# Kernel optimization log

Measured on AMD Instinct MI355X. Metric: run time of the kernel, lower is better.

Reference implementation:

```python
import jax, jax.numpy as jnp
import numpy as np

ALPHA = 0.9        # LIF membrane decay
THRESH = 1.0       # spike threshold
SURR_BETA = 4.0    # surrogate-gradient sharpness
TIME_STEPS = 32    # fabric simulation steps per token position


def _spike(v):
    """Heaviside spike with sigmoid surrogate gradient (straight-through)."""
    hard = (v >= THRESH).astype(v.dtype)
    soft = jax.nn.sigmoid(SURR_BETA * (v - THRESH))
    return soft + jax.lax.stop_gradient(hard - soft)


def setup_inputs() -> dict:
    key = jax.random.key(0)
    k0, k1, k2, k3 = jax.random.split(key, 4)
    B, S, D = 8, 128, 512
    N_in, N_out = 1024, 1024
    embeddings = jax.random.normal(k0, (B, S, D), jnp.float32)
    W_in = jax.random.normal(k1, (D, N_in), jnp.float32) / np.sqrt(D).astype(np.float32)
    b_in = jnp.zeros((N_in,), jnp.float32)
    W_conn = jax.random.normal(k2, (N_in, N_out), jnp.float32) / np.sqrt(N_in).astype(np.float32)
    W_out = jax.random.normal(k3, (N_out, D), jnp.float32) / np.sqrt(N_out).astype(np.float32)
    b_out = jnp.zeros((D,), jnp.float32)
    return {"embeddings": embeddings, "W_in": W_in, "b_in": b_in,
            "W_conn": W_conn, "W_out": W_out, "b_out": b_out}


def reference(embeddings, W_in, b_in, W_conn, W_out, b_out):
    B, S, D = embeddings.shape
    N_in = W_in.shape[1]
    N_out = W_conn.shape[1]

    # embed_to_snn + relu, precomputed for all positions: [B, S, N_in]
    snn_input = jax.nn.relu(jnp.einsum('bsd,dn->bsn', embeddings, W_in) + b_in)

    def time_step(carry, _):
        v_in, v_out, pos_input = carry
        # input population: leaky integrate external current
        v_in = ALPHA * v_in + pos_input
        s_in = _spike(v_in)
        v_in = v_in - s_in * THRESH          # soft reset
        # output population: driven by input-population spikes
        v_out = ALPHA * v_out + s_in @ W_conn
        s_out = _spike(v_out)
        v_out = v_out - s_out * THRESH
        n_spk = jax.lax.stop_gradient(s_in.sum() + s_out.sum())
        return (v_in, v_out, pos_input), (s_out, n_spk)

    def pos_step(carry, pos_input):
        v_in, v_out = carry
        (v_in, v_out, _), (s_outs, n_spks) = jax.lax.scan(
            time_step, (v_in, v_out, pos_input), None, length=TIME_STEPS)
        spike_acc = s_outs.sum(axis=0)       # [B, N_out], sum over timesteps
        pos_out = spike_acc @ W_out + b_out  # snn_to_embed
        return (v_in, v_out), (pos_out, n_spks.sum())

    v0_in = jnp.zeros((B, N_in), embeddings.dtype)
    v0_out = jnp.zeros((B, N_out), embeddings.dtype)
    snn_seq = jnp.swapaxes(snn_input, 0, 1)  # [S, B, N_in]: scan over positions
    _, (outs, spk_counts) = jax.lax.scan(pos_step, (v0_in, v0_out), snn_seq)

    output_embeddings = jnp.swapaxes(outs, 0, 1)  # [B, S, D]
    total_neurons = N_in + N_out
    spike_rate = spk_counts.sum() / (B * S * total_neurons * TIME_STEPS)
    return output_embeddings, spike_rate
```

## Files before the change

kernel.cpp:

```cpp
#include <hip/hip_runtime.h>
#include <stdint.h>

#define B 8
#define S 128
#define D 512
#define NIN 1024
#define NOUT 1024
#define T 32

typedef __attribute__((ext_vector_type(8))) short short8;
typedef __attribute__((ext_vector_type(4))) float floatx4;

__device__ __forceinline__ void gload_lds16(const void* g, void* l)
{
    __builtin_amdgcn_global_load_lds(
        (const __attribute__((address_space(1))) unsigned int*)g,
        (__attribute__((address_space(3))) unsigned int*)l,
        16, 0, 0);
}

__global__ __launch_bounds__(256) void k_gemm(const float* __restrict__ A,
                                              const float* __restrict__ Bm,
                                              const float* __restrict__ bias,
                                              float* __restrict__ C,
                                              int M, int N, int K, int relu)
{
    __shared__ float As[16][64];
    __shared__ float Bs[16][64];
    const int tid = threadIdx.x;
    const int bx = blockIdx.x, by = blockIdx.y;
    const int tx = tid & 15, ty = tid >> 4;
    const int ar = tid >> 2, ak = (tid & 3) << 2;
    const int bk = tid >> 4, bc = (tid & 15) << 2;
    float acc[4][4] = {{0.f,0.f,0.f,0.f},{0.f,0.f,0.f,0.f},
                       {0.f,0.f,0.f,0.f},{0.f,0.f,0.f,0.f}};
    float4 a4 = *(const float4*)(A + (size_t)(by*64 + ar)*K + ak);
    float4 b4 = *(const float4*)(Bm + (size_t)bk*N + bx*64 + bc);
    for (int k0 = 0; k0 < K; k0 += 16) {
        __syncthreads();
        As[ak+0][ar] = a4.x; As[ak+1][ar] = a4.y;
        As[ak+2][ar] = a4.z; As[ak+3][ar] = a4.w;
        *(float4*)&Bs[bk][bc] = b4;
        float4 na, nb;
        const bool has = (k0 + 16 < K);
        if (has) {
            na = *(const float4*)(A + (size_t)(by*64 + ar)*K + k0 + 16 + ak);
            nb = *(const float4*)(Bm + (size_t)(k0 + 16 + bk)*N + bx*64 + bc);
        }
        __syncthreads();
        #pragma unroll
        for (int kk = 0; kk < 16; ++kk) {
            float4 av = *(const float4*)&As[kk][ty << 2];
            float4 bv = *(const float4*)&Bs[kk][tx << 2];
            acc[0][0] = fmaf(av.x, bv.x, acc[0][0]);
            acc[0][1] = fmaf(av.x, bv.y, acc[0][1]);
            acc[0][2] = fmaf(av.x, bv.z, acc[0][2]);
            acc[0][3] = fmaf(av.x, bv.w, acc[0][3]);
            acc[1][0] = fmaf(av.y, bv.x, acc[1][0]);
            acc[1][1] = fmaf(av.y, bv.y, acc[1][1]);
            acc[1][2] = fmaf(av.y, bv.z, acc[1][2]);
            acc[1][3] = fmaf(av.y, bv.w, acc[1][3]);
            acc[2][0] = fmaf(av.z, bv.x, acc[2][0]);
            acc[2][1] = fmaf(av.z, bv.y, acc[2][1]);
            acc[2][2] = fmaf(av.z, bv.z, acc[2][2]);
            acc[2][3] = fmaf(av.z, bv.w, acc[2][3]);
            acc[3][0] = fmaf(av.w, bv.x, acc[3][0]);
            acc[3][1] = fmaf(av.w, bv.y, acc[3][1]);
            acc[3][2] = fmaf(av.w, bv.z, acc[3][2]);
            acc[3][3] = fmaf(av.w, bv.w, acc[3][3]);
        }
        if (has) { a4 = na; b4 = nb; }
    }
    const int row0 = by*64 + (ty << 2), col0 = bx*64 + (tx << 2);
    float4 bb = *(const float4*)(bias + col0);
    #pragma unroll
    for (int i = 0; i < 4; ++i) {
        float4 o;
        o.x = acc[i][0] + bb.x; o.y = acc[i][1] + bb.y;
        o.z = acc[i][2] + bb.z; o.w = acc[i][3] + bb.w;
        if (relu) {
            o.x = fmaxf(o.x, 0.f); o.y = fmaxf(o.y, 0.f);
            o.z = fmaxf(o.z, 0.f); o.w = fmaxf(o.w, 0.f);
        }
        *(float4*)(C + (size_t)(row0 + i)*N + col0) = o;
    }
}

__global__ __launch_bounds__(64) void k_lif_inA(const float* __restrict__ snn,
                                                unsigned int* __restrict__ sbits,
                                                unsigned int* __restrict__ counters)
{
    const int tid = blockIdx.x * 64 + threadIdx.x;
    const int b = tid >> 10, n = tid & (NIN - 1);
    const float* cur = snn + (size_t)(b * S) * NIN + n;
    float v = 0.f;
    int cnt = 0;
    float I   = cur[0];
    float In1 = (1 < S) ? cur[(size_t)1 * NIN] : 0.f;
    for (int s = 0; s < S; ++s) {
        const float In2 = (s + 2 < S) ? cur[(size_t)(s + 2) * NIN] : 0.f;
        unsigned int bits = 0u;
        #pragma unroll
        for (int t = 0; t < T; ++t) {
            v = __fadd_rn(__fmul_rn(0.9f, v), I);
            const bool sp = (v >= 1.0f);
            v = sp ? (v - 1.0f) : v;
            bits |= (sp ? 1u : 0u) << t;
        }
        sbits[(size_t)(b * S + s) * NIN + n] = bits;
        cnt += __popc(bits);
        I = In1; In1 = In2;
    }
    atomicAdd(counters, (unsigned int)cnt);
}

__global__ __launch_bounds__(256) void k_lif_inB(const unsigned int* __restrict__ sbits,
                                                 unsigned long long* __restrict__ masks)
{
    const int bs = blockIdx.x;
    const int w = threadIdx.x >> 6, lane = threadIdx.x & 63;
    #pragma unroll
    for (int i = 0; i < 4; ++i) {
        const int wq = w * 4 + i;
        const unsigned int bits = sbits[(size_t)bs * NIN + wq * 64 + lane];
        #pragma unroll
        for (int t = 0; t < T; ++t) {
            const unsigned long long m = __ballot((bits >> t) & 1u);
            if (lane == 0)
                masks[((size_t)bs * T + t) * 16 + wq] = m;
        }
    }
}

__global__ __launch_bounds__(256) void k_prep(const float* __restrict__ Wc,
                                              unsigned short* __restrict__ WhT,
                                              unsigned short* __restrict__ WlT)
{
    __shared__ float tile[64][65];
    const int k0 = blockIdx.x * 64, n0 = blockIdx.y * 64;
    const int tx = threadIdx.x & 63, ty = threadIdx.x >> 6;
    #pragma unroll
    for (int p = 0; p < 16; ++p) {
        const int kl = p*4 + ty;
        tile[kl][tx] = Wc[(size_t)(k0 + kl) * NOUT + n0 + tx];
    }
    __syncthreads();
    #pragma unroll
    for (int p = 0; p < 16; ++p) {
        const int nl = p*4 + ty;
        const float w = tile[tx][nl];
        const unsigned int u  = __float_as_uint(w);
        const unsigned int hb = (u + 0x7FFFu + ((u >> 16) & 1u)) & 0xFFFF0000u;
        const float hif = __uint_as_float(hb);
        const float lo  = w - hif;
        const unsigned int ul = __float_as_uint(lo);
        const unsigned short lob = (unsigned short)((ul + 0x7FFFu + ((ul >> 16) & 1u)) >> 16);
        WhT[(size_t)(n0 + nl) * NIN + k0 + tx] = (unsigned short)(hb >> 16);
        WlT[(size_t)(n0 + nl) * NIN + k0 + tx] = lob;
    }
}

__global__ __launch_bounds__(256) void k_conn_mfma(const uint4* __restrict__ masks128,
                                                   const unsigned short* __restrict__ WhT,
                                                   const unsigned short* __restrict__ WlT,
                                                   float* __restrict__ Iout,
                                                   int s0, int P)
{
    __shared__ unsigned short Bsm[2][2][64][128];

    const int tid = threadIdx.x;
    const int w = tid >> 6, lane = tid & 63;
    const int r16 = lane & 15, q = lane >> 4;
    const int PT = P * T;
    const int rowblk = blockIdx.x * 256 + w * 64;
    const int cb = blockIdx.y * 64;

    const uint4* aptr[4];
    #pragma unroll
    for (int f = 0; f < 4; ++f) {
        const int r = rowblk + f*16 + r16;
        const int b = r / PT;
        const int within = r - b * PT;
        const int grow = (b * S + s0) * T + within;
        aptr[f] = masks128 + (size_t)grow * 8;
    }

    const unsigned short* stg_src[8];
    #pragma unroll
    for (int i = 0; i < 8; ++i) {
        const int flat = tid + i * 256;
        const int mat  = flat >> 10;
        const int col  = (flat >> 4) & 63;
        const int k16  = flat & 15;
        const int k16s = k16 ^ (col & 7);
        stg_src[i] = (mat ? WlT : WhT) + (size_t)(cb + col) * NIN + k16s * 8;
    }

#define STAGE(BUF, CH) do {                                                   \
        char* dst0 = (char*)(&Bsm[BUF][0][0][0]) + (size_t)tid * 16;          \
        _Pragma("unroll")                                                     \
        for (int i_ = 0; i_ < 8; ++i_)                                        \
            gload_lds16(stg_src[i_] + (CH) * 128, dst0 + i_ * 4096);          \
    } while (0)

#define COMPUTE(BUF, AW) do {                                                 \
        _Pragma("unroll")                                                     \
        for (int kc = 0; kc < 4; ++kc) {                                      \
            short8 bh[4], bl[4];                                              \
            const int kread = ((kc*4 + q) ^ (r16 & 7)) * 8;                   \
            _Pragma("unroll")                                                 \
            for (int c = 0; c < 4; ++c) {                                     \
                bh[c] = *(const short8*)&Bsm[BUF][0][c*16 + r16][kread];      \
                bl[c] = *(const short8*)&Bsm[BUF][1][c*16 + r16][kread];      \
            }                                                                 \
            _Pragma("unroll")                                                 \
            for (int f = 0; f < 4; ++f) {                                     \
                const unsigned int word = (kc == 0) ? AW[f].x                 \
                                        : (kc == 1) ? AW[f].y                 \
                                        : (kc == 2) ? AW[f].z : AW[f].w;      \
                const unsigned int byte = (word >> (q * 8)) & 0xFFu;          \
                uint4 av_;                                                    \
                av_.x = ((byte &   1u) ? 0x3F80u : 0u)                        \
                      | ((byte &   2u) ? 0x3F800000u : 0u);                   \
                av_.y = ((byte &   4u) ? 0x3F80u : 0u)                        \
                      | ((byte &   8u) ? 0x3F800000u : 0u);                   \
                av_.z = ((byte &  16u) ? 0x3F80u : 0u)                        \
                      | ((byte &  32u) ? 0x3F800000u : 0u);                   \
                av_.w = ((byte &  64u) ? 0x3F80u : 0u)                        \
                      | ((byte & 128u) ? 0x3F800000u : 0u);                   \
                const short8 a = *(const short8*)&av_;                        \
                _Pragma("unroll")                                             \
                for (int c = 0; c < 4; ++c) {                                 \
                    acc[f][c] = __builtin_amdgcn_mfma_f32_16x16x32_bf16(      \
                                    a, bh[c], acc[f][c], 0, 0, 0);            \
                    acc[f][c] = __builtin_amdgcn_mfma_f32_16x16x32_bf16(      \
                                    a, bl[c], acc[f][c], 0, 0, 0);            \
                }                                                             \
            }                                                                 \
        }                                                                     \
    } while (0)

    floatx4 acc[4][4];
    #pragma unroll
    for (int f = 0; f < 4; ++f)
        #pragma unroll
        for (int c = 0; c < 4; ++c)
            acc[f][c] = (floatx4){0.f, 0.f, 0.f, 0.f};

    uint4 awA[4], awB[4];
    #pragma unroll
    for (int f = 0; f < 4; ++f) awA[f] = aptr[f][0];
    STAGE(0, 0);
    __syncthreads();

    #pragma unroll 1
    for (int ch = 0; ch < 8; ch += 2) {
        STAGE(1, ch + 1);
        #pragma unroll
        for (int f = 0; f < 4; ++f) awB[f] = aptr[f][ch + 1];
        COMPUTE(0, awA);
        __syncthreads();

        if (ch + 2 < 8) {
            STAGE(0, ch + 2);
            #pragma unroll
            for (int f = 0; f < 4; ++f) awA[f] = aptr[f][ch + 2];
        }
        COMPUTE(1, awB);
        __syncthreads();
    }
#undef STAGE
#undef COMPUTE

    #pragma unroll
    for (int f = 0; f < 4; ++f) {
        const int row = rowblk + f*16 + q*4;
        #pragma unroll
        for (int c = 0; c < 4; ++c) {
            const int col = cb + c*16 + r16;
            #pragma unroll
            for (int i = 0; i < 4; ++i)
                Iout[(size_t)(row + i) * NOUT + col] = acc[f][c][i];
        }
    }
}

__global__ __launch_bounds__(64) void k_lif_out(const float* __restrict__ Iout,
                                                float* __restrict__ vstate,
                                                float* __restrict__ sacc_out,
                                                unsigned int* __restrict__ counters,
                                                int s0, int P, int init)
{
    const int tid = blockIdx.x * 64 + threadIdx.x;
    const int b = tid >> 10, n = tid & (NOUT - 1);
    const int Tc = P * T;
    float v = init ? 0.f : vstate[tid];
    const float* ip = Iout + (size_t)b * Tc * NOUT + n;
    int cnt = 0;

    float cur[T], n1[T];
    #pragma unroll
    for (int t = 0; t < T; ++t) cur[t] = ip[(size_t)t * NOUT];
    if (1 < P) {
        const float* ip1 = ip + (size_t)T * NOUT;
        #pragma unroll
        for (int t = 0; t < T; ++t) n1[t] = ip1[(size_t)t * NOUT];
    }

    for (int sl = 0; sl < P; ++sl) {
        float n2[T];
        const bool has2 = (sl + 2 < P);
        if (has2) {
            const float* ip2 = ip + (size_t)(sl + 2) * T * NOUT;
            #pragma unroll
            for (int t = 0; t < T; ++t) n2[t] = ip2[(size_t)t * NOUT];
        }
        float sacc = 0.f;
        #pragma unroll
        for (int t = 0; t < T; ++t) {
            v = __fadd_rn(__fmul_rn(0.9f, v), cur[t]);
            const bool sp = (v >= 1.0f);
            v = sp ? (v - 1.0f) : v;
            sacc += sp ? 1.f : 0.f;
            cnt += sp ? 1 : 0;
        }
        sacc_out[(size_t)(b*S + s0 + sl) * NOUT + n] = sacc;
        if (sl + 1 < P) {
            #pragma unroll
            for (int t = 0; t < T; ++t) cur[t] = n1[t];
        }
        if (has2) {
            #pragma unroll
            for (int t = 0; t < T; ++t) n1[t] = n2[t];
        }
    }
    vstate[tid] = v;
    atomicAdd(counters + 1, (unsigned int)cnt);
}

__global__ void k_init(unsigned int* c)
{
    if (threadIdx.x < 2) c[threadIdx.x] = 0u;
}

__global__ void k_rate(const unsigned int* __restrict__ c, float* __restrict__ out)
{
    if (threadIdx.x == 0 && blockIdx.x == 0) {
        const float total = (float)c[0] + (float)c[1];
        out[0] = total / (float)(B * S * (NIN + NOUT) * T);
    }
}

extern "C" void kernel_launch(void* const* d_in, const int* in_sizes, int n_in,
                              void* d_out, int out_size, void* d_ws, size_t ws_size,
                              hipStream_t stream)
{
    const float* E    = (const float*)d_in[0];
    const float* Win  = (const float*)d_in[1];
    const float* bin  = (const float*)d_in[2];
    const float* Wc   = (const float*)d_in[3];
    const float* Wout = (const float*)d_in[4];
    const float* bout = (const float*)d_in[5];
    float* out = (float*)d_out;

    char* w = (char*)d_ws;
    float* snn              = (float*)(w);
    unsigned short* WhT     = (unsigned short*)(w);
    unsigned short* WlT     = (unsigned short*)(w + (2 << 20));
    unsigned long long* msk = (unsigned long long*)(w + (4 << 20));
    float* sacc             = (float*)(w + (8 << 20));
    unsigned int* sbits     = (unsigned int*)(w + (8 << 20));
    float* vst              = (float*)(w + (12 << 20));
    unsigned int* cnt       = (unsigned int*)(w + (12 << 20) + (64 << 10));
    float* Iout             = (float*)(w + (13 << 20));

    const size_t base = (size_t)13 << 20;
    const size_t avail = (ws_size > base) ? (ws_size - base) : 0;
    int P = 1;
    if      (avail >= (size_t)B * 128 * T * NOUT * 4) P = 128;
    else if (avail >= (size_t)B *  16 * T * NOUT * 4) P = 16;
    else if (avail >= (size_t)B *   4 * T * NOUT * 4) P = 4;

    k_init<<<1, 64, 0, stream>>>(cnt);

    dim3 g1(NIN / 64, (B * S) / 64);
    k_gemm<<<g1, 256, 0, stream>>>(E, Win, bin, snn, B * S, NIN, D, 1);

    k_lif_inA<<<128, 64, 0, stream>>>(snn, sbits, cnt);
    k_lif_inB<<<B * S, 256, 0, stream>>>(sbits, msk);

    dim3 gp(NIN / 64, NOUT / 64);
    k_prep<<<gp, 256, 0, stream>>>(Wc, WhT, WlT);

    for (int c = 0; c < S / P; ++c) {
        dim3 gc((B * P * T) / 256, NOUT / 64);
        k_conn_mfma<<<gc, 256, 0, stream>>>((const uint4*)msk, WhT, WlT, Iout, c * P, P);
        k_lif_out<<<128, 64, 0, stream>>>(Iout, vst, sacc, cnt, c * P, P, c == 0 ? 1 : 0);
    }

    dim3 g2(D / 64, (B * S) / 64);
    k_gemm<<<g2, 256, 0, stream>>>(sacc, Wout, bout, out, B * S, D, NOUT, 0);

    k_rate<<<1, 64, 0, stream>>>(cnt, out + (size_t)B * S * D);
}
```

Measured before the change: 442.2 us.

## Use LDS lookup table for spike-mask expansion and XCD-aware block remapping

```diff
diff --git a/kernel.cpp b/kernel.cpp
--- a/kernel.cpp
+++ b/kernel.cpp
@@ -166,14 +166,32 @@
                                                    float* __restrict__ Iout,
                                                    int s0, int P)
 {
+    __shared__ uint4 lut[256];
     __shared__ unsigned short Bsm[2][2][64][128];
 
     const int tid = threadIdx.x;
+    {
+        const unsigned int bb = (unsigned int)tid;
+        unsigned int r[4];
+        #pragma unroll
+        for (int i = 0; i < 4; ++i) {
+            const unsigned int b0 = (bb >> (2*i)) & 1u, b1 = (bb >> (2*i+1)) & 1u;
+            r[i] = (b0 ? 0x3F80u : 0u) | (b1 ? 0x3F800000u : 0u);
+        }
+        lut[tid] = make_uint4(r[0], r[1], r[2], r[3]);
+    }
+
+    const int bid = blockIdx.x + blockIdx.y * gridDim.x;
+    const int xcd = bid & 7;
+    const int j   = bid >> 3;
+    const int bxe = j & 127;
+    const int bye = 2 * xcd + (j >> 7);
+
     const int w = tid >> 6, lane = tid & 63;
     const int r16 = lane & 15, q = lane >> 4;
     const int PT = P * T;
-    const int rowblk = blockIdx.x * 256 + w * 64;
-    const int cb = blockIdx.y * 64;
+    const int rowblk = bxe * 256 + w * 64;
+    const int cb = bye * 64;
 
     const uint4* aptr[4];
     #pragma unroll
@@ -219,16 +237,7 @@
                                         : (kc == 1) ? AW[f].y                 \
                                         : (kc == 2) ? AW[f].z : AW[f].w;      \
                 const unsigned int byte = (word >> (q * 8)) & 0xFFu;          \
-                uint4 av_;                                                    \
-                av_.x = ((byte &   1u) ? 0x3F80u : 0u)                        \
-                      | ((byte &   2u) ? 0x3F800000u : 0u);                   \
-                av_.y = ((byte &   4u) ? 0x3F80u : 0u)                        \
-                      | ((byte &   8u) ? 0x3F800000u : 0u);                   \
-                av_.z = ((byte &  16u) ? 0x3F80u : 0u)                        \
-                      | ((byte &  32u) ? 0x3F800000u : 0u);                   \
-                av_.w = ((byte &  64u) ? 0x3F80u : 0u)                        \
-                      | ((byte & 128u) ? 0x3F800000u : 0u);                   \
-                const short8 a = *(const short8*)&av_;                        \
+                const short8 a = *(const short8*)&lut[byte];                  \
                 _Pragma("unroll")                                             \
                 for (int c = 0; c < 4; ++c) {                                 \
                     acc[f][c] = __builtin_amdgcn_mfma_f32_16x16x32_bf16(      \
```

Result: no change. 434.9 us (-1.7%).
